# Performance work log

Hardware: AMD Instinct MI355X
Metric: run time of the kernel (lower is better)

## Reference

```python
import jax, jax.numpy as jnp
from jax import lax
import numpy as np

T, D, H, E, K = 4096, 1024, 2048, 8, 2

def setup_inputs() -> dict:
    key = jax.random.key(0)
    ks = jax.random.split(key, 5)
    x = jax.random.normal(ks[0], (T, D), dtype=jnp.float32)
    weights = jax.random.uniform(ks[1], (T, K), dtype=jnp.float32)
    indices = jax.random.randint(ks[2], (T, K), 0, E, dtype=jnp.int64)
    # GatedMLP params (bias=False): fc1 weight [2H, D], fc2 weight [D, H], stacked over experts
    W1 = jax.random.normal(ks[3], (E, 2 * H, D), dtype=jnp.float32) * 0.02
    W2 = jax.random.normal(ks[4], (E, D, H), dtype=jnp.float32) * 0.02
    return {"x": x, "weights": weights, "indices": indices, "W1": W1, "W2": W2}

def reference(x, weights, indices, W1, W2):
    # Combine per-token routing weights into a per-(token, expert) weight matrix.
    # Tokens not routed to expert e get weight 0, so the dense per-expert GatedMLP
    # weighted-sum is mathematically identical to the gather->MLP->scatter-add loop.
    onehot = jax.nn.one_hot(indices, E, dtype=weights.dtype)        # [T, K, E]
    w_te = jnp.einsum('tke,tk->et', onehot, weights)                # [E, T]

    def body(y, carry):
        W1e, W2e, we = carry                                        # [2H,D], [D,H], [T]
        h = x @ W1e.T                                               # [T, 2H]
        u, gate = jnp.split(h, 2, axis=-1)                          # [T, H] each
        out = (u * jax.nn.silu(gate)) @ W2e.T                       # [T, D]
        return y + out * we[:, None], None

    y, _ = lax.scan(body, jnp.zeros_like(x), (W1, W2, w_te))
    return y
```

## Files before the change

### kernel.cpp

```cpp
#include <hip/hip_runtime.h>
#include <stdint.h>

#define T_TOK 4096
#define D_DIM 1024
#define H_DIM 2048
#define E_EXP 8
#define K_TOP 2
#define NTK   (T_TOK * K_TOP)
#define MT1 256
#define MAXT1 48

typedef short bf16x8 __attribute__((ext_vector_type(8)));
typedef float f32x4  __attribute__((ext_vector_type(4)));

#define MINI(a, b) ((a) < (b) ? (a) : (b))
#define MFMA_BF16 __builtin_amdgcn_mfma_f32_16x16x32_bf16

__device__ __forceinline__ unsigned short f2bf(float f) {
  unsigned u = __float_as_uint(f);
  u += 0x7fffu + ((u >> 16) & 1u);
  return (unsigned short)(u >> 16);
}

#define GLDS16(gp, lp)                                                        \
  __builtin_amdgcn_global_load_lds(                                           \
      (const __attribute__((address_space(1))) void*)(gp),                    \
      (__attribute__((address_space(3))) void*)(lp), 16, 0, 0)


#define NX8   (T_TOK * D_DIM / 8)
#define NW18  (E_EXP * 2 * H_DIM * D_DIM / 8)
#define NW28  (E_EXP * D_DIM * H_DIM / 8)
#define PRE_CVT_BLKS ((NX8 + NW18) / 256)
#define PRE_BLKS (PRE_CVT_BLKS + 32)

__global__ __launch_bounds__(256) void k_pre(const float* __restrict__ x,
                                             const float* __restrict__ W1,
                                             const int* __restrict__ idx,
                                             unsigned short* __restrict__ xb,
                                             unsigned short* __restrict__ W1b,
                                             int* __restrict__ meta) {
  int bid = blockIdx.x;
  int tid = threadIdx.x;
  if (bid >= PRE_CVT_BLKS) {
    __shared__ int h[E_EXP];
    if (tid < E_EXP) h[tid] = 0;
    __syncthreads();
    int i = (bid - PRE_CVT_BLKS) * 256 + tid;
    atomicAdd(&h[idx[i] & (E_EXP - 1)], 1);
    __syncthreads();
    if (tid < E_EXP) atomicAdd(&meta[tid], h[tid]);
    return;
  }
  long gid = (long)bid * 256 + tid;
  const float* src;
  unsigned short* dst;
  long i;
  if (gid < NX8) { src = x; dst = xb; i = gid; }
  else           { src = W1; dst = W1b; i = gid - NX8; }
  float4 a = ((const float4*)src)[2 * i];
  float4 b = ((const float4*)src)[2 * i + 1];
  uint4 o;
  o.x = f2bf(a.x) | ((unsigned)f2bf(a.y) << 16);
  o.y = f2bf(a.z) | ((unsigned)f2bf(a.w) << 16);
  o.z = f2bf(b.x) | ((unsigned)f2bf(b.y) << 16);
  o.w = f2bf(b.z) | ((unsigned)f2bf(b.w) << 16);
  ((uint4*)dst)[i] = o;
}

__global__ __launch_bounds__(256) void k_route_scatter(const int* __restrict__ idx,
                                                       const float* __restrict__ w,
                                                       int* __restrict__ meta,
                                                       unsigned short* __restrict__ rows,
                                                       unsigned short* __restrict__ slotpos,
                                                       float* __restrict__ wv) {
  __shared__ int h[E_EXP], base[E_EXP];
  int tid = threadIdx.x;
  if (tid < E_EXP) h[tid] = 0;
  __syncthreads();
  int i = blockIdx.x * 256 + tid;
  int e = idx[i] & (E_EXP - 1);
  int r = atomicAdd(&h[e], 1);
  __syncthreads();
  if (blockIdx.x == 0 && tid == 0) {
    int off = 0, nt = 0;
    for (int ee = 0; ee < E_EXP; ++ee) {
      int c = meta[ee];
      meta[176 + ee] = nt;
      for (int rr = 0; rr < c; rr += MT1) {
        meta[32 + nt]  = ee;
        meta[80 + nt]  = off + rr;
        meta[128 + nt] = MINI(MT1, c - rr);
        ++nt;
      }
      off += c;
    }
    meta[24]  = nt;
    meta[184] = nt;
  }
  if (tid < E_EXP) {
    int off = 0;
#pragma unroll
    for (int ee = 0; ee < E_EXP; ++ee)
      if (ee < tid) off += meta[ee];
    base[tid] = off + atomicAdd(&meta[16 + tid], h[tid]);
  }
  __syncthreads();
  int p = base[e] + r;
  rows[p]    = (unsigned short)(i >> 1);
  slotpos[i] = (unsigned short)p;
  wv[p]      = w[i];
}

#define G1_TILES (MAXT1 * 32)
#define CVW2_BLK 1024
#define G1_GRID  (G1_TILES + CVW2_BLK)

__global__ __launch_bounds__(256, 2) void k_gemm1(
    const unsigned short* __restrict__ xb,
    const unsigned short* __restrict__ W1b,
    const int* __restrict__ meta,
    const unsigned short* __restrict__ rows,
    const float* __restrict__ wv,
    unsigned short* __restrict__ act,
    const float* __restrict__ W2,
    unsigned short* __restrict__ W2b) {
  int bid = blockIdx.x;
  int tid = threadIdx.x;

  if (bid >= G1_TILES) {
    long g0 = (long)(bid - G1_TILES) * 256 + tid;
    for (long i = g0; i < NW28; i += (long)CVW2_BLK * 256) {
      float4 a = ((const float4*)W2)[2 * i];
      float4 b = ((const float4*)W2)[2 * i + 1];
      uint4 o;
      o.x = f2bf(a.x) | ((unsigned)f2bf(a.y) << 16);
      o.y = f2bf(a.z) | ((unsigned)f2bf(a.w) << 16);
      o.z = f2bf(b.x) | ((unsigned)f2bf(b.y) << 16);
      o.w = f2bf(b.z) | ((unsigned)f2bf(b.w) << 16);
      ((uint4*)W2b)[i] = o;
    }
    return;
  }

  int nt = meta[24];
  int tb = bid % MAXT1;
  int y  = bid / MAXT1;
  if (tb >= nt) return;
  int e     = meta[32 + tb];
  int r0    = meta[80 + tb];
  int valid = meta[128 + tb];
  int n0    = y << 6;

  __shared__ unsigned short lA[256 * 64];
  __shared__ unsigned short lB1[64 * 64];
  __shared__ unsigned short lB2[64 * 64];
  __shared__ float sw[256];

  int wave = tid >> 6, lane = tid & 63;

  sw[tid] = wv[r0 + MINI(tid, valid - 1)];

  const unsigned short* w1e = W1b + (size_t)e * (4096 * 1024);

  const unsigned short *pA[8], *pB1[2], *pB2[2];
#pragma unroll
  for (int it = 0; it < 8; ++it) {
    int c = it * 256 + tid;
    int r = c >> 3, cc = c & 7;
    int g = cc ^ (r & 7);
    int tok = rows[r0 + MINI(r, valid - 1)];
    pA[it] = xb + (size_t)tok * 1024 + g * 8;
  }
#pragma unroll
  for (int it = 0; it < 2; ++it) {
    int c = it * 256 + tid;
    int r = c >> 3, cc = c & 7;
    int g = cc ^ (r & 7);
    pB1[it] = w1e + (size_t)(n0 + r) * 1024 + g * 8;
    pB2[it] = w1e + (size_t)(2048 + n0 + r) * 1024 + g * 8;
  }

  f32x4 zero = {0.f, 0.f, 0.f, 0.f};
  f32x4 au[4][4], ag[4][4];
#pragma unroll
  for (int i = 0; i < 4; ++i)
#pragma unroll
    for (int j = 0; j < 4; ++j) { au[i][j] = zero; ag[i][j] = zero; }

  int mb = wave * 64;
  int fr = lane & 15, q = lane >> 4;

  for (int k0 = 0; k0 < 1024; k0 += 64) {
    __syncthreads();
#pragma unroll
    for (int it = 0; it < 8; ++it)
      GLDS16(pA[it] + k0, &lA[(it * 256 + wave * 64) * 8]);
#pragma unroll
    for (int it = 0; it < 2; ++it) {
      int lb = (it * 256 + wave * 64) * 8;
      GLDS16(pB1[it] + k0, &lB1[lb]);
      GLDS16(pB2[it] + k0, &lB2[lb]);
    }
    __syncthreads();
#pragma unroll
    for (int kk = 0; kk < 2; ++kk) {
      int co = (((kk << 2) + q) ^ (fr & 7)) * 8 + fr * 64;
      bf16x8 a[4];
#pragma unroll
      for (int i = 0; i < 4; ++i)
        a[i] = *(const bf16x8*)&lA[(mb + i * 16) * 64 + co];
#pragma unroll
      for (int j = 0; j < 4; ++j) {
        bf16x8 bu = *(const bf16x8*)&lB1[(j * 16) * 64 + co];
        bf16x8 bg = *(const bf16x8*)&lB2[(j * 16) * 64 + co];
#pragma unroll
        for (int i = 0; i < 4; ++i) {
          au[i][j] = MFMA_BF16(a[i], bu, au[i][j], 0, 0, 0);
          ag[i][j] = MFMA_BF16(a[i], bg, ag[i][j], 0, 0, 0);
        }
      }
    }
  }

#pragma unroll
  for (int i = 0; i < 4; ++i) {
#pragma unroll
    for (int reg = 0; reg < 4; ++reg) {
      int lm = mb + i * 16 + q * 4 + reg;
      if (lm < valid) {
        float wrow = sw[lm];
        size_t orow = (size_t)(r0 + lm) * 2048;
#pragma unroll
        for (int j = 0; j < 4; ++j) {
          float u = au[i][j][reg];
          float g = ag[i][j][reg];
          float s = g / (1.f + __expf(-g));
          act[orow + (n0 + j * 16 + fr)] = f2bf(u * s * wrow);
        }
      }
    }
  }
}

#define G2_GRID (E_EXP * 8 * 32)

__global__ __launch_bounds__(256, 2) void k_gemm2(
    const unsigned short* __restrict__ act,
    const unsigned short* __restrict__ W2b,
    const int* __restrict__ meta,
    float* __restrict__ y) {
  int bid = blockIdx.x;
  int e  = bid & 7;
  int s  = bid >> 3;
  int ti = s >> 3;
  int yy = s & 7;
  int ts  = meta[176 + e];
  int ntl = meta[177 + e] - ts;
  if (ti >= ntl) return;
  int tb    = ts + ti;
  int r0    = meta[80 + tb];
  int valid = meta[128 + tb];
  int n0    = yy << 7;

  __shared__ unsigned short lA[256 * 64];
  __shared__ unsigned short lB[128 * 64];

  int tid = threadIdx.x;
  int wave = tid >> 6, lane = tid & 63;

  const unsigned short* w2e = W2b + (size_t)e * (1024 * 2048);

  const unsigned short *pA[8], *pB[4];
#pragma unroll
  for (int it = 0; it < 8; ++it) {
    int c = it * 256 + tid;
    int r = c >> 3, cc = c & 7;
    int g = cc ^ (r & 7);
    pA[it] = act + (size_t)(r0 + MINI(r, valid - 1)) * 2048 + g * 8;
  }
#pragma unroll
  for (int it = 0; it < 4; ++it) {
    int c = it * 256 + tid;
    int r = c >> 3, cc = c & 7;
    int g = cc ^ (r & 7);
    pB[it] = w2e + (size_t)(n0 + r) * 2048 + g * 8;
  }

  f32x4 zero = {0.f, 0.f, 0.f, 0.f};
  f32x4 acc[4][8];
#pragma unroll
  for (int i = 0; i < 4; ++i)
#pragma unroll
    for (int j = 0; j < 8; ++j) acc[i][j] = zero;

  int mb = wave * 64;
  int fr = lane & 15, q = lane >> 4;

  for (int k0 = 0; k0 < 2048; k0 += 64) {
    __syncthreads();
#pragma unroll
    for (int it = 0; it < 8; ++it)
      GLDS16(pA[it] + k0, &lA[(it * 256 + wave * 64) * 8]);
#pragma unroll
    for (int it = 0; it < 4; ++it)
      GLDS16(pB[it] + k0, &lB[(it * 256 + wave * 64) * 8]);
    __syncthreads();
#pragma unroll
    for (int kk = 0; kk < 2; ++kk) {
      int co = (((kk << 2) + q) ^ (fr & 7)) * 8 + fr * 64;
      bf16x8 a[4];
#pragma unroll
      for (int i = 0; i < 4; ++i)
        a[i] = *(const bf16x8*)&lA[(mb + i * 16) * 64 + co];
#pragma unroll
      for (int j = 0; j < 8; ++j) {
        bf16x8 b = *(const bf16x8*)&lB[(j * 16) * 64 + co];
#pragma unroll
        for (int i = 0; i < 4; ++i)
          acc[i][j] = MFMA_BF16(a[i], b, acc[i][j], 0, 0, 0);
      }
    }
  }

#pragma unroll
  for (int i = 0; i < 4; ++i) {
#pragma unroll
    for (int reg = 0; reg < 4; ++reg) {
      int lm = mb + i * 16 + q * 4 + reg;
      if (lm < valid) {
        float* yp = y + (size_t)(r0 + lm) * 1024 + n0;
#pragma unroll
        for (int j = 0; j < 8; ++j)
          yp[j * 16 + fr] = acc[i][j][reg];
      }
    }
  }
}

__global__ __launch_bounds__(256) void k_combine(
    const float* __restrict__ y,
    const unsigned short* __restrict__ slotpos,
    float* __restrict__ out) {
  int t = blockIdx.x;
  int s0 = slotpos[2 * t], s1 = slotpos[2 * t + 1];
  const float4* a = (const float4*)(y + (size_t)s0 * 1024);
  const float4* b = (const float4*)(y + (size_t)s1 * 1024);
  float4* o = (float4*)(out + (size_t)t * 1024);
  int d = threadIdx.x;
  float4 va = a[d], vb = b[d];
  float4 vo = {va.x + vb.x, va.y + vb.y, va.z + vb.z, va.w + vb.w};
  o[d] = vo;
}

extern "C" void kernel_launch(void* const* d_in, const int* in_sizes, int n_in,
                              void* d_out, int out_size, void* d_ws, size_t ws_size,
                              hipStream_t stream) {
  const float* x  = (const float*)d_in[0];
  const float* w  = (const float*)d_in[1];
  const int*  idx = (const int*)d_in[2];
  const float* W1 = (const float*)d_in[3];
  const float* W2 = (const float*)d_in[4];
  float* out = (float*)d_out;

  char* ws = (char*)d_ws;
  unsigned short* W1b = (unsigned short*)(ws);
  float*          yslot = (float*)(ws);
  unsigned short* W2b = (unsigned short*)(ws + 67108864);
  unsigned short* xb  = (unsigned short*)(ws + 100663296);
  unsigned short* act = (unsigned short*)(ws + 109051904);
  unsigned short* rows    = (unsigned short*)(ws + 142606336);
  unsigned short* slotpos = (unsigned short*)(ws + 142622720);
  float* wv   = (float*)(ws + 142639104);
  int*   meta = (int*)(ws + 142671872);

  hipMemsetAsync(meta, 0, 1024, stream);

  k_pre<<<PRE_BLKS, 256, 0, stream>>>(x, W1, idx, xb, W1b, meta);
  k_route_scatter<<<32, 256, 0, stream>>>(idx, w, meta, rows, slotpos, wv);

  k_gemm1<<<G1_GRID, 256, 0, stream>>>(xb, W1b, meta, rows, wv, act, W2, W2b);

  k_gemm2<<<G2_GRID, 256, 0, stream>>>(act, W2b, meta, yslot);

  k_combine<<<T_TOK, 256, 0, stream>>>(yslot, slotpos, out);
}
```

Measured before the change: 412.8 us.

## Split-K the second expert GEMM over a flat tile list, reduce in combine

k_gemm2 now walks the flat list of expert tiles (up to 40) instead of a sparse per-expert grid. It also splits the 2048-long K dimension into two halves, each block writing partial sums to a separate y buffer. k_combine sums four partial rows per token instead of two. This raises block count and cuts wasted early-exit blocks, at the cost of double the fp32 intermediate writes and reads.

Result: slower. 421.1 us (+2.0%).

```diff
diff --git a/kernel.cpp b/kernel.cpp
--- a/kernel.cpp
+++ b/kernel.cpp
@@ -86,7 +86,6 @@
     int off = 0, nt = 0;
     for (int ee = 0; ee < E_EXP; ++ee) {
       int c = meta[ee];
-      meta[176 + ee] = nt;
       for (int rr = 0; rr < c; rr += MT1) {
         meta[32 + nt]  = ee;
         meta[80 + nt]  = off + rr;
@@ -95,8 +94,7 @@
       }
       off += c;
     }
-    meta[24]  = nt;
-    meta[184] = nt;
+    meta[24] = nt;
   }
   if (tid < E_EXP) {
     int off = 0;
@@ -243,7 +241,8 @@
   }
 }
 
-#define G2_GRID (E_EXP * 8 * 32)
+#define G2_TILES 40
+#define G2_GRID (G2_TILES * 8 * 2)
 
 __global__ __launch_bounds__(256, 2) void k_gemm2(
     const unsigned short* __restrict__ act,
@@ -251,17 +250,17 @@
     const int* __restrict__ meta,
     float* __restrict__ y) {
   int bid = blockIdx.x;
-  int e  = bid & 7;
-  int s  = bid >> 3;
-  int ti = s >> 3;
-  int yy = s & 7;
-  int ts  = meta[176 + e];
-  int ntl = meta[177 + e] - ts;
-  if (ti >= ntl) return;
-  int tb    = ts + ti;
+  int kz = bid & 1;
+  int s  = bid >> 1;
+  int tb = s % G2_TILES;
+  int yy = s / G2_TILES;
+  int nt = meta[24];
+  if (tb >= nt) return;
+  int e     = meta[32 + tb];
   int r0    = meta[80 + tb];
   int valid = meta[128 + tb];
   int n0    = yy << 7;
+  int kbase = kz << 10;
 
   __shared__ unsigned short lA[256 * 64];
   __shared__ unsigned short lB[128 * 64];
@@ -277,14 +276,14 @@
     int c = it * 256 + tid;
     int r = c >> 3, cc = c & 7;
     int g = cc ^ (r & 7);
-    pA[it] = act + (size_t)(r0 + MINI(r, valid - 1)) * 2048 + g * 8;
+    pA[it] = act + (size_t)(r0 + MINI(r, valid - 1)) * 2048 + kbase + g * 8;
   }
 #pragma unroll
   for (int it = 0; it < 4; ++it) {
     int c = it * 256 + tid;
     int r = c >> 3, cc = c & 7;
     int g = cc ^ (r & 7);
-    pB[it] = w2e + (size_t)(n0 + r) * 2048 + g * 8;
+    pB[it] = w2e + (size_t)(n0 + r) * 2048 + kbase + g * 8;
   }
 
   f32x4 zero = {0.f, 0.f, 0.f, 0.f};
@@ -297,7 +296,7 @@
   int mb = wave * 64;
   int fr = lane & 15, q = lane >> 4;
 
-  for (int k0 = 0; k0 < 2048; k0 += 64) {
+  for (int k0 = 0; k0 < 1024; k0 += 64) {
     __syncthreads();
 #pragma unroll
     for (int it = 0; it < 8; ++it)
@@ -323,13 +322,14 @@
     }
   }
 
+  float* yk = y + (size_t)kz * (NTK * 1024);
 #pragma unroll
   for (int i = 0; i < 4; ++i) {
 #pragma unroll
     for (int reg = 0; reg < 4; ++reg) {
       int lm = mb + i * 16 + q * 4 + reg;
       if (lm < valid) {
-        float* yp = y + (size_t)(r0 + lm) * 1024 + n0;
+        float* yp = yk + (size_t)(r0 + lm) * 1024 + n0;
 #pragma unroll
         for (int j = 0; j < 8; ++j)
           yp[j * 16 + fr] = acc[i][j][reg];
@@ -344,12 +344,15 @@
     float* __restrict__ out) {
   int t = blockIdx.x;
   int s0 = slotpos[2 * t], s1 = slotpos[2 * t + 1];
-  const float4* a = (const float4*)(y + (size_t)s0 * 1024);
-  const float4* b = (const float4*)(y + (size_t)s1 * 1024);
+  const float4* a0 = (const float4*)(y + (size_t)s0 * 1024);
+  const float4* a1 = (const float4*)(y + (size_t)(NTK + s0) * 1024);
+  const float4* b0 = (const float4*)(y + (size_t)s1 * 1024);
+  const float4* b1 = (const float4*)(y + (size_t)(NTK + s1) * 1024);
   float4* o = (float4*)(out + (size_t)t * 1024);
   int d = threadIdx.x;
-  float4 va = a[d], vb = b[d];
-  float4 vo = {va.x + vb.x, va.y + vb.y, va.z + vb.z, va.w + vb.w};
+  float4 va = a0[d], vb = a1[d], vc = b0[d], vd = b1[d];
+  float4 vo = {va.x + vb.x + vc.x + vd.x, va.y + vb.y + vc.y + vd.y,
+               va.z + vb.z + vc.z + vd.z, va.w + vb.w + vc.w + vd.w};
   o[d] = vo;
 }
 
```

## Shrink GEMM2 M-tile to 128 rows with compact tile list and 2x2 wave layout

Applied to the files above, without the earlier changes.

GEMM2 now uses its own 128-row tile list built in the routing kernel instead of the 256-row tiles shared with GEMM1. The grid is indexed over a compact list of tiles rather than a sparse expert-by-slot layout that launched many blocks only to exit early. Waves are arranged 2x2 over a 128x128 output tile, which halves the accumulators and the A-tile LDS. The aim is less padding waste, more useful blocks and better occupancy, at the cost of loading each W2 tile about twice as often.

Result: no change. 417.4 us (+1.1%).

```diff
diff --git a/kernel.cpp b/kernel.cpp
--- a/kernel.cpp
+++ b/kernel.cpp
@@ -8,7 +8,9 @@
 #define K_TOP 2
 #define NTK   (T_TOK * K_TOP)
 #define MT1 256
+#define MT2 128
 #define MAXT1 48
+#define MAXT2 72
 
 typedef short bf16x8 __attribute__((ext_vector_type(8)));
 typedef float f32x4  __attribute__((ext_vector_type(4)));
@@ -83,20 +85,25 @@
   int r = atomicAdd(&h[e], 1);
   __syncthreads();
   if (blockIdx.x == 0 && tid == 0) {
-    int off = 0, nt = 0;
+    int off = 0, nt1 = 0, nt2 = 0;
     for (int ee = 0; ee < E_EXP; ++ee) {
       int c = meta[ee];
-      meta[176 + ee] = nt;
       for (int rr = 0; rr < c; rr += MT1) {
-        meta[32 + nt]  = ee;
-        meta[80 + nt]  = off + rr;
-        meta[128 + nt] = MINI(MT1, c - rr);
-        ++nt;
+        meta[32 + nt1]  = ee;
+        meta[80 + nt1]  = off + rr;
+        meta[128 + nt1] = MINI(MT1, c - rr);
+        ++nt1;
+      }
+      for (int rr = 0; rr < c; rr += MT2) {
+        meta[192 + nt2] = ee;
+        meta[264 + nt2] = off + rr;
+        meta[336 + nt2] = MINI(MT2, c - rr);
+        ++nt2;
       }
       off += c;
     }
-    meta[24]  = nt;
-    meta[184] = nt;
+    meta[24] = nt1;
+    meta[25] = nt2;
   }
   if (tid < E_EXP) {
     int off = 0;
@@ -243,7 +250,7 @@
   }
 }
 
-#define G2_GRID (E_EXP * 8 * 32)
+#define G2_GRID (MAXT2 * 8)
 
 __global__ __launch_bounds__(256, 2) void k_gemm2(
     const unsigned short* __restrict__ act,
@@ -251,60 +258,51 @@
     const int* __restrict__ meta,
     float* __restrict__ y) {
   int bid = blockIdx.x;
-  int e  = bid & 7;
-  int s  = bid >> 3;
-  int ti = s >> 3;
-  int yy = s & 7;
-  int ts  = meta[176 + e];
-  int ntl = meta[177 + e] - ts;
-  if (ti >= ntl) return;
-  int tb    = ts + ti;
-  int r0    = meta[80 + tb];
-  int valid = meta[128 + tb];
+  int tb = bid % MAXT2;
+  int yy = bid / MAXT2;
+  int nt2 = meta[25];
+  if (tb >= nt2) return;
+  int e     = meta[192 + tb];
+  int r0    = meta[264 + tb];
+  int valid = meta[336 + tb];
   int n0    = yy << 7;
 
-  __shared__ unsigned short lA[256 * 64];
+  __shared__ unsigned short lA[128 * 64];
   __shared__ unsigned short lB[128 * 64];
 
   int tid = threadIdx.x;
   int wave = tid >> 6, lane = tid & 63;
+  int wm = wave >> 1, wn = wave & 1;
 
   const unsigned short* w2e = W2b + (size_t)e * (1024 * 2048);
 
-  const unsigned short *pA[8], *pB[4];
-#pragma unroll
-  for (int it = 0; it < 8; ++it) {
+  const unsigned short *pA[4], *pB[4];
+#pragma unroll
+  for (int it = 0; it < 4; ++it) {
     int c = it * 256 + tid;
     int r = c >> 3, cc = c & 7;
     int g = cc ^ (r & 7);
     pA[it] = act + (size_t)(r0 + MINI(r, valid - 1)) * 2048 + g * 8;
-  }
-#pragma unroll
-  for (int it = 0; it < 4; ++it) {
-    int c = it * 256 + tid;
-    int r = c >> 3, cc = c & 7;
-    int g = cc ^ (r & 7);
     pB[it] = w2e + (size_t)(n0 + r) * 2048 + g * 8;
   }
 
   f32x4 zero = {0.f, 0.f, 0.f, 0.f};
-  f32x4 acc[4][8];
+  f32x4 acc[4][4];
 #pragma unroll
   for (int i = 0; i < 4; ++i)
 #pragma unroll
-    for (int j = 0; j < 8; ++j) acc[i][j] = zero;
-
-  int mb = wave * 64;
+    for (int j = 0; j < 4; ++j) acc[i][j] = zero;
+
+  int mb = wm * 64, nb = wn * 64;
   int fr = lane & 15, q = lane >> 4;
 
   for (int k0 = 0; k0 < 2048; k0 += 64) {
     __syncthreads();
 #pragma unroll
-    for (int it = 0; it < 8; ++it)
+    for (int it = 0; it < 4; ++it) {
       GLDS16(pA[it] + k0, &lA[(it * 256 + wave * 64) * 8]);
-#pragma unroll
-    for (int it = 0; it < 4; ++it)
       GLDS16(pB[it] + k0, &lB[(it * 256 + wave * 64) * 8]);
+    }
     __syncthreads();
 #pragma unroll
     for (int kk = 0; kk < 2; ++kk) {
@@ -314,8 +312,8 @@
       for (int i = 0; i < 4; ++i)
         a[i] = *(const bf16x8*)&lA[(mb + i * 16) * 64 + co];
 #pragma unroll
-      for (int j = 0; j < 8; ++j) {
-        bf16x8 b = *(const bf16x8*)&lB[(j * 16) * 64 + co];
+      for (int j = 0; j < 4; ++j) {
+        bf16x8 b = *(const bf16x8*)&lB[(nb + j * 16) * 64 + co];
 #pragma unroll
         for (int i = 0; i < 4; ++i)
           acc[i][j] = MFMA_BF16(a[i], b, acc[i][j], 0, 0, 0);
@@ -329,9 +327,9 @@
     for (int reg = 0; reg < 4; ++reg) {
       int lm = mb + i * 16 + q * 4 + reg;
       if (lm < valid) {
-        float* yp = y + (size_t)(r0 + lm) * 1024 + n0;
-#pragma unroll
-        for (int j = 0; j < 8; ++j)
+        float* yp = y + (size_t)(r0 + lm) * 1024 + n0 + nb;
+#pragma unroll
+        for (int j = 0; j < 4; ++j)
           yp[j * 16 + fr] = acc[i][j][reg];
       }
     }
@@ -374,7 +372,7 @@
   float* wv   = (float*)(ws + 142639104);
   int*   meta = (int*)(ws + 142671872);
 
-  hipMemsetAsync(meta, 0, 1024, stream);
+  hipMemsetAsync(meta, 0, 2048, stream);
 
   k_pre<<<PRE_BLKS, 256, 0, stream>>>(x, W1, idx, xb, W1b, meta);
   k_route_scatter<<<32, 256, 0, stream>>>(idx, w, meta, rows, slotpos, wv);
```
